# Kernel tuning notes

Hardware: AMD Instinct MI355X
Metric: run time of the kernel (lower is better)

The kernel has to match this reference:

```python
import jax, jax.numpy as jnp
import numpy as np

P = 5            # NumberOfParameters
M = 20           # NumberOfNetworks = (2+P)(1+P)/2 - 1
N = 131072       # events
K = 64           # parameter hypotheses
D = 16           # input features (AR[0])
H = 64           # hidden width (AR[1]=AR[2])


def setup_inputs() -> dict:
    key = jax.random.key(0)
    ks = jax.random.split(key, 8)
    return {
        "Data": jax.random.normal(ks[0], (N, D), jnp.float32),
        "Parameters": jax.random.normal(ks[1], (K, P), jnp.float32),
        "Shift": jax.random.normal(ks[2], (D,), jnp.float32),
        "Scaling": jnp.ones((D,), jnp.float32),
        "ParameterScaling": jnp.ones((P,), jnp.float32),
        "W1": jax.random.normal(ks[3], (M, H, D), jnp.float32) * (1.0 / np.sqrt(D)),
        "b1": jax.random.normal(ks[4], (M, H), jnp.float32) * 0.01,
        "W2": jax.random.normal(ks[5], (M, H, H), jnp.float32) * (1.0 / np.sqrt(H)),
        "b2": jax.random.normal(ks[6], (M, H), jnp.float32) * 0.01,
        "W3": jax.random.normal(ks[7], (M, H), jnp.float32) * (1.0 / np.sqrt(H)),
        "b3": jnp.zeros((M,), jnp.float32),
    }


def reference(Data, Parameters, Shift, Scaling, ParameterScaling, W1, b1, W2, b2, W3, b3):
    Pp1 = P + 1
    # Preprocess (torch.no_grad -> stop_gradient)
    x = jax.lax.stop_gradient((Data - Shift) / Scaling)            # [N, D]
    par = jax.lax.stop_gradient(Parameters / ParameterScaling)     # [K, P]

    # All M tiny MLPs batched: ReLU(Linear) x2 then Linear -> scalar per event
    h = jax.nn.relu(jnp.einsum('nd,mhd->mnh', x, W1) + b1[:, None, :])   # [M, N, H]
    h = jax.nn.relu(jnp.einsum('mnh,mgh->mng', h, W2) + b2[:, None, :])  # [M, N, H]
    out = jnp.einsum('mnh,mh->mn', h, W3) + b3[:, None]                  # [M, N]

    # MatrixLT: entry (0,0) = 1, networks fill remaining upper-triangular
    # entries in row-major order (matches the torch EntryIterator loop).
    rows, cols = np.triu_indices(Pp1)
    flat = rows * Pp1 + cols                      # static indices; flat[0] == 0
    Mlt = jnp.zeros((x.shape[0], Pp1 * Pp1), x.dtype)
    Mlt = Mlt.at[:, flat[0]].set(1.0)
    Mlt = Mlt.at[:, flat[1:]].set(out.T)          # [N, (P+1)^2]
    Mlt = Mlt.reshape(-1, Pp1, Pp1)               # [N, P+1, P+1]

    # ParMatrix = [1, theta] per hypothesis
    ParM = jnp.concatenate([jnp.ones((par.shape[0], 1), par.dtype), par], axis=1)  # [K, P+1]

    MltP = jnp.einsum('bij,kj->bik', Mlt, ParM)   # [N, P+1, K]
    rho = jnp.einsum('bik,bik->bk', MltP, MltP)   # [N, K]
    return rho
```

## Files before the change

### kernel.cpp

```cpp
#include <hip/hip_runtime.h>

typedef float    f32x4  __attribute__((ext_vector_type(4)));
typedef float    f32x16 __attribute__((ext_vector_type(16)));
typedef __bf16   bf16x8 __attribute__((ext_vector_type(8)));
typedef __bf16   bf16x2 __attribute__((ext_vector_type(2)));
typedef unsigned uint2v __attribute__((ext_vector_type(2)));
typedef unsigned u32x4  __attribute__((ext_vector_type(4)));

union Frag { unsigned u[4]; bf16x8 b; };

static __device__ __forceinline__ unsigned pack2(float a, float b) {
    bf16x2 t;
    t[0] = (__bf16)a;
    t[1] = (__bf16)b;
    return __builtin_bit_cast(unsigned, t);
}

static __device__ __forceinline__ unsigned relupk(float a, float b, unsigned zero) {
    unsigned x = pack2(a, b), r;
    asm("v_pk_max_f16 %0, %1, %2" : "=v"(r) : "v"(x), "v"(zero));
    return r;
}

static __device__ __forceinline__ unsigned short f2bfu(float x) {
    __bf16 b = (__bf16)x;
    return __builtin_bit_cast(unsigned short, b);
}

static __device__ __forceinline__ float bflo(unsigned u) { return __builtin_bit_cast(float, u << 16); }
static __device__ __forceinline__ float bfhi(unsigned u) { return __builtin_bit_cast(float, u & 0xffff0000u); }

static __device__ __forceinline__ uint2v pswap(unsigned a, unsigned b) {
#if __has_builtin(__builtin_amdgcn_permlane32_swap)
    return __builtin_amdgcn_permlane32_swap(a, b, false, false);
#else
    unsigned ax = (unsigned)__shfl_xor((int)a, 32);
    unsigned bx = (unsigned)__shfl_xor((int)b, 32);
    bool lo = (__lane_id() & 32) == 0;
    uint2v r;
    r[0] = lo ? a : bx;
    r[1] = lo ? ax : b;
    return r;
#endif
}

static __device__ __forceinline__ float xhalf_sum(float s, int half) {
    unsigned su = __builtin_bit_cast(unsigned, s);
    uint2v r = pswap(su, su);
    float other = __builtin_bit_cast(float, half ? r[0] : r[1]);
    return s + other;
}

__global__ __launch_bounds__(256, 4) void prep_kernel(
    const float* __restrict__ W1, const float* __restrict__ W2,
    const float* __restrict__ b1, const float* __restrict__ b2,
    const float* __restrict__ W3,
    unsigned short* __restrict__ w1bf, unsigned short* __restrict__ w2f,
    float* __restrict__ w3f,
    unsigned* __restrict__ b1p, unsigned* __restrict__ b2p)
{
    const int t = blockIdx.x * 256 + threadIdx.x;
    if (t < 20480) w1bf[t] = f2bfu(W1[t]);
    if (t < 81920) {
        const int j = t & 7, l = (t >> 3) & 63, f = (t >> 9) & 7, m = t >> 12;
        const int g = 32 * (f >> 2) + (l & 31);
        const int h = 16 * (f & 3) + 8 * (l >> 5) + j;
        w2f[t] = f2bfu(W2[(m * 64 + g) * 64 + h]);
    }
    if (t < 1280) {
        const int i = t & 15, hf = (t >> 4) & 1, tt = (t >> 5) & 1, m = t >> 6;
        const int h = 32 * tt + 4 * hf + (i & 3) + 8 * (i >> 2);
        w3f[t] = W3[m * 64 + h];
    }
    if (t < 640) {
        const int q = t & 7, hf = (t >> 3) & 1, tt = (t >> 4) & 1, m = t >> 5;
        const int h0 = 32 * tt + 4 * hf + ((2 * q) & 3) + 8 * ((2 * q) >> 2);
        b1p[t] = pack2(b1[m * 64 + h0], b1[m * 64 + h0 + 1]);
        b2p[t] = pack2(b2[m * 64 + h0], b2[m * 64 + h0 + 1]);
    }
}

__global__ __launch_bounds__(256, 2) void fused_kernel(
    const unsigned short* __restrict__ w1bf,
    const unsigned short* __restrict__ w2f,
    const float* __restrict__ w3f,
    const unsigned* __restrict__ b1p,
    const unsigned* __restrict__ b2p,
    const float* __restrict__ b3,
    const float* __restrict__ Data,
    const float* __restrict__ Shift,
    const float* __restrict__ Scaling,
    const float* __restrict__ Parameters,
    const float* __restrict__ PScal,
    float* __restrict__ rho, int N)
{
    __shared__ float o[256][24];

    const int tid  = threadIdx.x;
    const int wave = tid >> 6;
    const int lane = tid & 63;
    const int ln   = lane & 31;
    const int half = lane >> 5;
    const int eb   = blockIdx.x;
    const int n0   = eb * 256;

    unsigned zero = 0;
    asm volatile("" : "+v"(zero));

    float sh[8], is[8];
    #pragma unroll
    for (int j = 0; j < 8; ++j) {
        sh[j] = Shift[8 * half + j];
        is[j] = 1.0f / Scaling[8 * half + j];
    }
    bf16x8 xf[8];
    #pragma unroll
    for (int f = 0; f < 8; ++f) {
        const float* dp = Data + (size_t)(n0 + 32 * f + ln) * 16 + 8 * half;
        f32x4 v0 = *(const f32x4*)dp;
        f32x4 v1 = *(const f32x4*)(dp + 4);
        float xv[8];
        #pragma unroll
        for (int j = 0; j < 4; ++j) {
            xv[j]     = (v0[j] - sh[j])     * is[j];
            xv[4 + j] = (v1[j] - sh[4 + j]) * is[4 + j];
        }
        Frag fx;
        #pragma unroll
        for (int c = 0; c < 4; ++c) fx.u[c] = pack2(xv[2 * c], xv[2 * c + 1]);
        xf[f] = fx.b;
    }

    const float pk1 = Parameters[lane * 5 + 0] / PScal[0];
    const float pk2 = Parameters[lane * 5 + 1] / PScal[1];
    const float pk3 = Parameters[lane * 5 + 2] / PScal[2];
    const float pk4 = Parameters[lane * 5 + 3] / PScal[3];
    const float pk5 = Parameters[lane * 5 + 4] / PScal[4];

    for (int mi = 0; mi < 5; ++mi) {
        const int m = wave * 5 + mi;
        bf16x8 a1[2];
        #pragma unroll
        for (int t = 0; t < 2; ++t)
            a1[t] = *(const bf16x8*)(w1bf + (size_t)(m * 64 + 32 * t + ln) * 16 + 8 * half);
        bf16x8 a2[8];
        #pragma unroll
        for (int f = 0; f < 8; ++f)
            a2[f] = *(const bf16x8*)(w2f + (size_t)((m * 8 + f) * 64 + lane) * 8);
        f32x16 w3r[2];
        #pragma unroll
        for (int t = 0; t < 2; ++t)
            w3r[t] = *(const f32x16*)(w3f + ((m * 2 + t) * 2 + half) * 16);
        const float b3v = b3[m];
        u32x4 b1r[2][2], b2r[2][2];
        #pragma unroll
        for (int t = 0; t < 2; ++t) {
            const unsigned* p1 = b1p + ((m * 2 + t) * 2 + half) * 8;
            b1r[t][0] = *(const u32x4*)p1;
            b1r[t][1] = *(const u32x4*)(p1 + 4);
            const unsigned* p2 = b2p + ((m * 2 + t) * 2 + half) * 8;
            b2r[t][0] = *(const u32x4*)p2;
            b2r[t][1] = *(const u32x4*)(p2 + 4);
        }

        #pragma unroll
        for (int it = 0; it < 2; ++it) {
            float res[4];
            #pragma unroll
            for (int e = 0; e < 4; ++e) {
                const bf16x8 xfe = xf[it * 4 + e];
                unsigned bfr[4][4];
                #pragma unroll
                for (int t = 0; t < 2; ++t) {
                    f32x16 acc;
                    #pragma unroll
                    for (int hq = 0; hq < 2; ++hq)
                        #pragma unroll
                        for (int q4 = 0; q4 < 4; ++q4) {
                            const unsigned u = b1r[t][hq][q4];
                            acc[8 * hq + 2 * q4]     = bflo(u);
                            acc[8 * hq + 2 * q4 + 1] = bfhi(u);
                        }
                    acc = __builtin_amdgcn_mfma_f32_32x32x16_bf16(a1[t], xfe, acc, 0, 0, 0);
                    unsigned p[8];
                    #pragma unroll
                    for (int q = 0; q < 8; ++q)
                        p[q] = relupk(acc[2 * q], acc[2 * q + 1], zero);
                    uint2v r0 = pswap(p[0], p[2]);
                    uint2v r1 = pswap(p[1], p[3]);
                    uint2v r2 = pswap(p[4], p[6]);
                    uint2v r3 = pswap(p[5], p[7]);
                    bfr[2 * t    ][0] = r0[0]; bfr[2 * t    ][1] = r1[0];
                    bfr[2 * t    ][2] = r0[1]; bfr[2 * t    ][3] = r1[1];
                    bfr[2 * t + 1][0] = r2[0]; bfr[2 * t + 1][1] = r3[0];
                    bfr[2 * t + 1][2] = r2[1]; bfr[2 * t + 1][3] = r3[1];
                }
                Frag fb[4];
                #pragma unroll
                for (int kk = 0; kk < 4; ++kk)
                    #pragma unroll
                    for (int c = 0; c < 4; ++c) fb[kk].u[c] = bfr[kk][c];
                f32x16 ac0, ac1;
                #pragma unroll
                for (int hq = 0; hq < 2; ++hq)
                    #pragma unroll
                    for (int q4 = 0; q4 < 4; ++q4) {
                        const unsigned u0 = b2r[0][hq][q4];
                        const unsigned u1 = b2r[1][hq][q4];
                        ac0[8 * hq + 2 * q4]     = bflo(u0);
                        ac0[8 * hq + 2 * q4 + 1] = bfhi(u0);
                        ac1[8 * hq + 2 * q4]     = bflo(u1);
                        ac1[8 * hq + 2 * q4 + 1] = bfhi(u1);
                    }
                #pragma unroll
                for (int kk = 0; kk < 4; ++kk) {
                    ac0 = __builtin_amdgcn_mfma_f32_32x32x16_bf16(a2[kk],     fb[kk].b, ac0, 0, 0, 0);
                    ac1 = __builtin_amdgcn_mfma_f32_32x32x16_bf16(a2[4 + kk], fb[kk].b, ac1, 0, 0, 0);
                }
                float s0 = 0.f, s1 = 0.f, s2 = 0.f, s3 = 0.f;
                #pragma unroll
                for (int q = 0; q < 4; ++q) {
                    s0 = fmaf(w3r[0][4 * q + 0], fmaxf(ac0[4 * q + 0], 0.f), s0);
                    s1 = fmaf(w3r[0][4 * q + 1], fmaxf(ac0[4 * q + 1], 0.f), s1);
                    s2 = fmaf(w3r[0][4 * q + 2], fmaxf(ac0[4 * q + 2], 0.f), s2);
                    s3 = fmaf(w3r[0][4 * q + 3], fmaxf(ac0[4 * q + 3], 0.f), s3);
                    s0 = fmaf(w3r[1][4 * q + 0], fmaxf(ac1[4 * q + 0], 0.f), s0);
                    s1 = fmaf(w3r[1][4 * q + 1], fmaxf(ac1[4 * q + 1], 0.f), s1);
                    s2 = fmaf(w3r[1][4 * q + 2], fmaxf(ac1[4 * q + 2], 0.f), s2);
                    s3 = fmaf(w3r[1][4 * q + 3], fmaxf(ac1[4 * q + 3], 0.f), s3);
                }
                const float s = (s0 + s1) + (s2 + s3);
                res[e] = xhalf_sum(s, half) + b3v;
            }
            o[it * 128 + lane][m]      = half ? res[1] : res[0];
            o[it * 128 + 64 + lane][m] = half ? res[3] : res[2];
        }
    }

    __syncthreads();

    #pragma unroll 4
    for (int i = 0; i < 64; ++i) {
        const int ev = wave * 64 + i;
        const f32x4* rr = (const f32x4*)&o[ev][0];
        f32x4 oa = rr[0], ob = rr[1], oc = rr[2], od = rr[3], oe = rr[4];
        float m0 = 1.0f + oa[0] * pk1 + oa[1] * pk2 + oa[2] * pk3 + oa[3] * pk4 + ob[0] * pk5;
        float m1 = ob[1] * pk1 + ob[2] * pk2 + ob[3] * pk3 + oc[0] * pk4 + oc[1] * pk5;
        float m2 = oc[2] * pk2 + oc[3] * pk3 + od[0] * pk4 + od[1] * pk5;
        float m3 = od[2] * pk3 + od[3] * pk4 + oe[0] * pk5;
        float m4 = oe[1] * pk4 + oe[2] * pk5;
        float m5 = oe[3] * pk5;
        float v = m0 * m0 + m1 * m1 + m2 * m2 + m3 * m3 + m4 * m4 + m5 * m5;
        rho[(size_t)(n0 + ev) * 64 + lane] = v;
    }
}

extern "C" void kernel_launch(void* const* d_in, const int* in_sizes, int n_in,
                              void* d_out, int out_size, void* d_ws, size_t ws_size,
                              hipStream_t stream)
{
    const float* Data   = (const float*)d_in[0];
    const float* Params = (const float*)d_in[1];
    const float* Shift  = (const float*)d_in[2];
    const float* Scal   = (const float*)d_in[3];
    const float* PScal  = (const float*)d_in[4];
    const float* W1     = (const float*)d_in[5];
    const float* b1     = (const float*)d_in[6];
    const float* W2     = (const float*)d_in[7];
    const float* b2     = (const float*)d_in[8];
    const float* W3     = (const float*)d_in[9];
    const float* b3     = (const float*)d_in[10];
    float* rho = (float*)d_out;
    const int N = in_sizes[0] / 16;

    char* ws = (char*)d_ws;
    unsigned short* w1bf = (unsigned short*)(ws);
    unsigned short* w2f  = (unsigned short*)(ws + 40960);
    unsigned*       b1p  = (unsigned*)(ws + 204800);
    unsigned*       b2p  = (unsigned*)(ws + 207360);
    float*          w3f  = (float*)(ws + 209920);

    prep_kernel<<<320, 256, 0, stream>>>(W1, W2, b1, b2, W3, w1bf, w2f, w3f, b1p, b2p);
    fused_kernel<<<N / 256, 256, 0, stream>>>(w1bf, w2f, w3f, b1p, b2p, b3,
                                              Data, Shift, Scal, Params, PScal, rho, N);
}
```

Before: 57.21 us.

## Halve events per block, pack W3 as bf16, raise occupancy to three blocks

Each block now processes 128 events instead of 256, so the per-thread input fragments and the shared output buffer shrink by half and the grid doubles. W3 is stored as packed bf16 pairs instead of fp32 to cut its register footprint, and the launch bound goes from 2 to 3 blocks per CU. The aim is more resident waves to hide MFMA and memory latency. The cost is that weights are reloaded per 128 events instead of per 256, and W3 loses precision.

```diff
diff --git a/kernel.cpp b/kernel.cpp
--- a/kernel.cpp
+++ b/kernel.cpp
@@ -56,8 +56,8 @@
     const float* __restrict__ b1, const float* __restrict__ b2,
     const float* __restrict__ W3,
     unsigned short* __restrict__ w1bf, unsigned short* __restrict__ w2f,
-    float* __restrict__ w3f,
-    unsigned* __restrict__ b1p, unsigned* __restrict__ b2p)
+    unsigned* __restrict__ b1p, unsigned* __restrict__ b2p,
+    unsigned* __restrict__ w3p)
 {
     const int t = blockIdx.x * 256 + threadIdx.x;
     if (t < 20480) w1bf[t] = f2bfu(W1[t]);
@@ -67,25 +67,21 @@
         const int h = 16 * (f & 3) + 8 * (l >> 5) + j;
         w2f[t] = f2bfu(W2[(m * 64 + g) * 64 + h]);
     }
-    if (t < 1280) {
-        const int i = t & 15, hf = (t >> 4) & 1, tt = (t >> 5) & 1, m = t >> 6;
-        const int h = 32 * tt + 4 * hf + (i & 3) + 8 * (i >> 2);
-        w3f[t] = W3[m * 64 + h];
-    }
     if (t < 640) {
         const int q = t & 7, hf = (t >> 3) & 1, tt = (t >> 4) & 1, m = t >> 5;
         const int h0 = 32 * tt + 4 * hf + ((2 * q) & 3) + 8 * ((2 * q) >> 2);
         b1p[t] = pack2(b1[m * 64 + h0], b1[m * 64 + h0 + 1]);
         b2p[t] = pack2(b2[m * 64 + h0], b2[m * 64 + h0 + 1]);
-    }
-}
-
-__global__ __launch_bounds__(256, 2) void fused_kernel(
+        w3p[t] = pack2(W3[m * 64 + h0], W3[m * 64 + h0 + 1]);
+    }
+}
+
+__global__ __launch_bounds__(256, 3) void fused_kernel(
     const unsigned short* __restrict__ w1bf,
     const unsigned short* __restrict__ w2f,
-    const float* __restrict__ w3f,
     const unsigned* __restrict__ b1p,
     const unsigned* __restrict__ b2p,
+    const unsigned* __restrict__ w3p,
     const float* __restrict__ b3,
     const float* __restrict__ Data,
     const float* __restrict__ Shift,
@@ -94,41 +90,42 @@
     const float* __restrict__ PScal,
     float* __restrict__ rho, int N)
 {
-    __shared__ float o[256][24];
+    __shared__ float o[128][24];
 
     const int tid  = threadIdx.x;
     const int wave = tid >> 6;
     const int lane = tid & 63;
     const int ln   = lane & 31;
     const int half = lane >> 5;
-    const int eb   = blockIdx.x;
-    const int n0   = eb * 256;
+    const int n0   = blockIdx.x * 128;
 
     unsigned zero = 0;
     asm volatile("" : "+v"(zero));
 
-    float sh[8], is[8];
-    #pragma unroll
-    for (int j = 0; j < 8; ++j) {
-        sh[j] = Shift[8 * half + j];
-        is[j] = 1.0f / Scaling[8 * half + j];
-    }
-    bf16x8 xf[8];
-    #pragma unroll
-    for (int f = 0; f < 8; ++f) {
-        const float* dp = Data + (size_t)(n0 + 32 * f + ln) * 16 + 8 * half;
-        f32x4 v0 = *(const f32x4*)dp;
-        f32x4 v1 = *(const f32x4*)(dp + 4);
-        float xv[8];
-        #pragma unroll
-        for (int j = 0; j < 4; ++j) {
-            xv[j]     = (v0[j] - sh[j])     * is[j];
-            xv[4 + j] = (v1[j] - sh[4 + j]) * is[4 + j];
-        }
-        Frag fx;
-        #pragma unroll
-        for (int c = 0; c < 4; ++c) fx.u[c] = pack2(xv[2 * c], xv[2 * c + 1]);
-        xf[f] = fx.b;
+    bf16x8 xf[4];
+    {
+        float sh[8], is[8];
+        #pragma unroll
+        for (int j = 0; j < 8; ++j) {
+            sh[j] = Shift[8 * half + j];
+            is[j] = 1.0f / Scaling[8 * half + j];
+        }
+        #pragma unroll
+        for (int f = 0; f < 4; ++f) {
+            const float* dp = Data + (size_t)(n0 + 32 * f + ln) * 16 + 8 * half;
+            f32x4 v0 = *(const f32x4*)dp;
+            f32x4 v1 = *(const f32x4*)(dp + 4);
+            float xv[8];
+            #pragma unroll
+            for (int j = 0; j < 4; ++j) {
+                xv[j]     = (v0[j] - sh[j])     * is[j];
+                xv[4 + j] = (v1[j] - sh[4 + j]) * is[4 + j];
+            }
+            Frag fx;
+            #pragma unroll
+            for (int c = 0; c < 4; ++c) fx.u[c] = pack2(xv[2 * c], xv[2 * c + 1]);
+            xf[f] = fx.b;
+        }
     }
 
     const float pk1 = Parameters[lane * 5 + 0] / PScal[0];
@@ -147,11 +144,7 @@
         #pragma unroll
         for (int f = 0; f < 8; ++f)
             a2[f] = *(const bf16x8*)(w2f + (size_t)((m * 8 + f) * 64 + lane) * 8);
-        f32x16 w3r[2];
-        #pragma unroll
-        for (int t = 0; t < 2; ++t)
-            w3r[t] = *(const f32x16*)(w3f + ((m * 2 + t) * 2 + half) * 16);
-        const float b3v = b3[m];
+        u32x4 w3u[2][2];
         u32x4 b1r[2][2], b2r[2][2];
         #pragma unroll
         for (int t = 0; t < 2; ++t) {
@@ -161,87 +154,92 @@
             const unsigned* p2 = b2p + ((m * 2 + t) * 2 + half) * 8;
             b2r[t][0] = *(const u32x4*)p2;
             b2r[t][1] = *(const u32x4*)(p2 + 4);
-        }
-
-        #pragma unroll
-        for (int it = 0; it < 2; ++it) {
-            float res[4];
-            #pragma unroll
-            for (int e = 0; e < 4; ++e) {
-                const bf16x8 xfe = xf[it * 4 + e];
-                unsigned bfr[4][4];
-                #pragma unroll
-                for (int t = 0; t < 2; ++t) {
-                    f32x16 acc;
-                    #pragma unroll
-                    for (int hq = 0; hq < 2; ++hq)
-                        #pragma unroll
-                        for (int q4 = 0; q4 < 4; ++q4) {
-                            const unsigned u = b1r[t][hq][q4];
-                            acc[8 * hq + 2 * q4]     = bflo(u);
-                            acc[8 * hq + 2 * q4 + 1] = bfhi(u);
-                        }
-                    acc = __builtin_amdgcn_mfma_f32_32x32x16_bf16(a1[t], xfe, acc, 0, 0, 0);
-                    unsigned p[8];
-                    #pragma unroll
-                    for (int q = 0; q < 8; ++q)
-                        p[q] = relupk(acc[2 * q], acc[2 * q + 1], zero);
-                    uint2v r0 = pswap(p[0], p[2]);
-                    uint2v r1 = pswap(p[1], p[3]);
-                    uint2v r2 = pswap(p[4], p[6]);
-                    uint2v r3 = pswap(p[5], p[7]);
-                    bfr[2 * t    ][0] = r0[0]; bfr[2 * t    ][1] = r1[0];
-                    bfr[2 * t    ][2] = r0[1]; bfr[2 * t    ][3] = r1[1];
-                    bfr[2 * t + 1][0] = r2[0]; bfr[2 * t + 1][1] = r3[0];
-                    bfr[2 * t + 1][2] = r2[1]; bfr[2 * t + 1][3] = r3[1];
-                }
-                Frag fb[4];
-                #pragma unroll
-                for (int kk = 0; kk < 4; ++kk)
-                    #pragma unroll
-                    for (int c = 0; c < 4; ++c) fb[kk].u[c] = bfr[kk][c];
-                f32x16 ac0, ac1;
+            const unsigned* p3 = w3p + ((m * 2 + t) * 2 + half) * 8;
+            w3u[t][0] = *(const u32x4*)p3;
+            w3u[t][1] = *(const u32x4*)(p3 + 4);
+        }
+        const float b3v = b3[m];
+
+        float res[4];
+        #pragma unroll
+        for (int e = 0; e < 4; ++e) {
+            const bf16x8 xfe = xf[e];
+            unsigned bfr[4][4];
+            #pragma unroll
+            for (int t = 0; t < 2; ++t) {
+                f32x16 acc;
                 #pragma unroll
                 for (int hq = 0; hq < 2; ++hq)
                     #pragma unroll
                     for (int q4 = 0; q4 < 4; ++q4) {
-                        const unsigned u0 = b2r[0][hq][q4];
-                        const unsigned u1 = b2r[1][hq][q4];
-                        ac0[8 * hq + 2 * q4]     = bflo(u0);
-                        ac0[8 * hq + 2 * q4 + 1] = bfhi(u0);
-                        ac1[8 * hq + 2 * q4]     = bflo(u1);
-                        ac1[8 * hq + 2 * q4 + 1] = bfhi(u1);
+                        const unsigned u = b1r[t][hq][q4];
+                        acc[8 * hq + 2 * q4]     = bflo(u);
+                        acc[8 * hq + 2 * q4 + 1] = bfhi(u);
                     }
-                #pragma unroll
-                for (int kk = 0; kk < 4; ++kk) {
-                    ac0 = __builtin_amdgcn_mfma_f32_32x32x16_bf16(a2[kk],     fb[kk].b, ac0, 0, 0, 0);
-                    ac1 = __builtin_amdgcn_mfma_f32_32x32x16_bf16(a2[4 + kk], fb[kk].b, ac1, 0, 0, 0);
+                acc = __builtin_amdgcn_mfma_f32_32x32x16_bf16(a1[t], xfe, acc, 0, 0, 0);
+                unsigned p[8];
+                #pragma unroll
+                for (int q = 0; q < 8; ++q)
+                    p[q] = relupk(acc[2 * q], acc[2 * q + 1], zero);
+                uint2v r0 = pswap(p[0], p[2]);
+                uint2v r1 = pswap(p[1], p[3]);
+                uint2v r2 = pswap(p[4], p[6]);
+                uint2v r3 = pswap(p[5], p[7]);
+                bfr[2 * t    ][0] = r0[0]; bfr[2 * t    ][1] = r1[0];
+                bfr[2 * t    ][2] = r0[1]; bfr[2 * t    ][3] = r1[1];
+                bfr[2 * t + 1][0] = r2[0]; bfr[2 * t + 1][1] = r3[0];
+                bfr[2 * t + 1][2] = r2[1]; bfr[2 * t + 1][3] = r3[1];
+            }
+            Frag fb[4];
+            #pragma unroll
+            for (int kk = 0; kk < 4; ++kk)
+                #pragma unroll
+                for (int c = 0; c < 4; ++c) fb[kk].u[c] = bfr[kk][c];
+            f32x16 ac0, ac1;
+            #pragma unroll
+            for (int hq = 0; hq < 2; ++hq)
+                #pragma unroll
+                for (int q4 = 0; q4 < 4; ++q4) {
+                    const unsigned u0 = b2r[0][hq][q4];
+                    const unsigned u1 = b2r[1][hq][q4];
+                    ac0[8 * hq + 2 * q4]     = bflo(u0);
+                    ac0[8 * hq + 2 * q4 + 1] = bfhi(u0);
+                    ac1[8 * hq + 2 * q4]     = bflo(u1);
+                    ac1[8 * hq + 2 * q4 + 1] = bfhi(u1);
                 }
-                float s0 = 0.f, s1 = 0.f, s2 = 0.f, s3 = 0.f;
-                #pragma unroll
-                for (int q = 0; q < 4; ++q) {
-                    s0 = fmaf(w3r[0][4 * q + 0], fmaxf(ac0[4 * q + 0], 0.f), s0);
-                    s1 = fmaf(w3r[0][4 * q + 1], fmaxf(ac0[4 * q + 1], 0.f), s1);
-                    s2 = fmaf(w3r[0][4 * q + 2], fmaxf(ac0[4 * q + 2], 0.f), s2);
-                    s3 = fmaf(w3r[0][4 * q + 3], fmaxf(ac0[4 * q + 3], 0.f), s3);
-                    s0 = fmaf(w3r[1][4 * q + 0], fmaxf(ac1[4 * q + 0], 0.f), s0);
-                    s1 = fmaf(w3r[1][4 * q + 1], fmaxf(ac1[4 * q + 1], 0.f), s1);
-                    s2 = fmaf(w3r[1][4 * q + 2], fmaxf(ac1[4 * q + 2], 0.f), s2);
-                    s3 = fmaf(w3r[1][4 * q + 3], fmaxf(ac1[4 * q + 3], 0.f), s3);
-                }
-                const float s = (s0 + s1) + (s2 + s3);
-                res[e] = xhalf_sum(s, half) + b3v;
-            }
-            o[it * 128 + lane][m]      = half ? res[1] : res[0];
-            o[it * 128 + 64 + lane][m] = half ? res[3] : res[2];
-        }
+            #pragma unroll
+            for (int kk = 0; kk < 4; ++kk) {
+                ac0 = __builtin_amdgcn_mfma_f32_32x32x16_bf16(a2[kk],     fb[kk].b, ac0, 0, 0, 0);
+                ac1 = __builtin_amdgcn_mfma_f32_32x32x16_bf16(a2[4 + kk], fb[kk].b, ac1, 0, 0, 0);
+            }
+            float s0 = 0.f, s1 = 0.f, s2 = 0.f, s3 = 0.f;
+            #pragma unroll
+            for (int q = 0; q < 4; ++q) {
+                const unsigned da = w3u[0][q >> 1][(2 * q) & 3];
+                const unsigned db = w3u[0][q >> 1][(2 * q + 1) & 3];
+                const unsigned dc = w3u[1][q >> 1][(2 * q) & 3];
+                const unsigned dd = w3u[1][q >> 1][(2 * q + 1) & 3];
+                s0 = fmaf(bflo(da), fmaxf(ac0[4 * q + 0], 0.f), s0);
+                s1 = fmaf(bfhi(da), fmaxf(ac0[4 * q + 1], 0.f), s1);
+                s2 = fmaf(bflo(db), fmaxf(ac0[4 * q + 2], 0.f), s2);
+                s3 = fmaf(bfhi(db), fmaxf(ac0[4 * q + 3], 0.f), s3);
+                s0 = fmaf(bflo(dc), fmaxf(ac1[4 * q + 0], 0.f), s0);
+                s1 = fmaf(bfhi(dc), fmaxf(ac1[4 * q + 1], 0.f), s1);
+                s2 = fmaf(bflo(dd), fmaxf(ac1[4 * q + 2], 0.f), s2);
+                s3 = fmaf(bfhi(dd), fmaxf(ac1[4 * q + 3], 0.f), s3);
+            }
+            const float s = (s0 + s1) + (s2 + s3);
+            res[e] = xhalf_sum(s, half) + b3v;
+        }
+        o[lane][m]      = half ? res[1] : res[0];
+        o[64 + lane][m] = half ? res[3] : res[2];
     }
 
     __syncthreads();
 
     #pragma unroll 4
-    for (int i = 0; i < 64; ++i) {
-        const int ev = wave * 64 + i;
+    for (int i = 0; i < 32; ++i) {
+        const int ev = wave * 32 + i;
         const f32x4* rr = (const f32x4*)&o[ev][0];
         f32x4 oa = rr[0], ob = rr[1], oc = rr[2], od = rr[3], oe = rr[4];
         float m0 = 1.0f + oa[0] * pk1 + oa[1] * pk2 + oa[2] * pk3 + oa[3] * pk4 + ob[0] * pk5;
@@ -278,9 +276,9 @@
     unsigned short* w2f  = (unsigned short*)(ws + 40960);
     unsigned*       b1p  = (unsigned*)(ws + 204800);
     unsigned*       b2p  = (unsigned*)(ws + 207360);
-    float*          w3f  = (float*)(ws + 209920);
-
-    prep_kernel<<<320, 256, 0, stream>>>(W1, W2, b1, b2, W3, w1bf, w2f, w3f, b1p, b2p);
-    fused_kernel<<<N / 256, 256, 0, stream>>>(w1bf, w2f, w3f, b1p, b2p, b3,
+    unsigned*       w3p  = (unsigned*)(ws + 209920);
+
+    prep_kernel<<<320, 256, 0, stream>>>(W1, W2, b1, b2, W3, w1bf, w2f, b1p, b2p, w3p);
+    fused_kernel<<<N / 128, 256, 0, stream>>>(w1bf, w2f, b1p, b2p, w3p, b3,
                                               Data, Shift, Scal, Params, PScal, rho, N);
 }
```

Measured after the change: 132.5 us. 132% more time.
